# Kernel optimization log

Hardware: AMD Instinct MI355X
Metric: run time of the kernel (lower is better)

## Reference

```python
import jax, jax.numpy as jnp
import numpy as np

EPS = 1e-5  # matches `self.dist(f, pt) + 1e-05` in the torch module

N, D, P = 262144, 64, 256


def setup_inputs() -> dict:
    key = jax.random.key(0)
    k1, k2, k3 = jax.random.split(key, 3)
    features = jax.random.normal(k1, (N, D), dtype=jnp.float32)      # flattened boxes' feature vectors
    prototypes = jax.random.normal(k2, (P, D), dtype=jnp.float32)    # stacked self.prototypes.values()
    proto_labels = jax.random.randint(k3, (P,), 0, 1000)             # list(self.prototypes) keys
    return {"features": features, "prototypes": prototypes, "proto_labels": proto_labels}


def reference(features, prototypes, proto_labels):
    # F.mse_loss(f, pt) = mean((f - pt)**2) over the D feature dim.
    # Expand ||f - p||^2 = ||f||^2 - 2 f.p + ||p||^2 so we never materialize [N, P, D].
    d = features.shape[-1]
    f2 = jnp.sum(features * features, axis=-1, keepdims=True)          # [N, 1]
    p2 = jnp.sum(prototypes * prototypes, axis=-1)                     # [P]
    cross = features @ prototypes.T                                    # [N, P]
    mse = (f2 - 2.0 * cross + p2[None, :]) / d                         # [N, P] per-pair MSE
    inv_d = 1.0 / (mse + EPS)                                          # ds in the torch code
    labels = proto_labels[jnp.argmax(inv_d, axis=-1)]                  # box[-1] = fls[ds.argmax()]
    return inv_d, labels
```

## Files before the change

kernel.cpp:

```cpp
#include <hip/hip_runtime.h>


#define PROTOS 256
#define DIM 64
#define MARGIN 0.125f

__global__ __launch_bounds__(256, 4)
void protonet_kernel(const float* __restrict__ feats,
                     const float* __restrict__ protos,
                     const int* __restrict__ plabels,
                     float* __restrict__ out_inv,
                     float* __restrict__ out_lab,
                     int rows_total)
{
    const int p    = threadIdx.x;
    const int lane = threadIdx.x & 63;
    const int wid  = threadIdx.x >> 6;

    float pr[DIM];
    {
        const float4* prv = (const float4*)(protos + p * DIM);
        #pragma unroll
        for (int i = 0; i < DIM / 4; ++i) {
            float4 v = prv[i];
            pr[4 * i + 0] = v.x; pr[4 * i + 1] = v.y;
            pr[4 * i + 2] = v.z; pr[4 * i + 3] = v.w;
        }
    }
    double p2d = 0.0;
    #pragma unroll
    for (int k = 0; k < DIM; ++k) p2d = fma((double)pr[k], (double)pr[k], p2d);
    float p2f = (float)p2d;

    __shared__ unsigned int s_m1[4], s_m2[4];
    __shared__ double s_dval[4];
    __shared__ int    s_didx[4];
    __shared__ int    s_flag;

    for (int row = blockIdx.x; row < rows_total; row += gridDim.x) {
        const float* frow = feats + (size_t)row * DIM;
        const float4* f4  = (const float4*)frow;

        float fv  = frow[lane];
        float fsf = fv * fv;
        #pragma unroll
        for (int s = 32; s > 0; s >>= 1) fsf += __shfl_xor(fsf, s, 64);

        float a0 = 0.f, a1 = 0.f, a2 = 0.f, a3 = 0.f;
        #pragma unroll
        for (int i = 0; i < DIM / 4; ++i) {
            float4 x = f4[i];
            a0 = fmaf(x.x, pr[4 * i + 0], a0);
            a1 = fmaf(x.y, pr[4 * i + 1], a1);
            a2 = fmaf(x.z, pr[4 * i + 2], a2);
            a3 = fmaf(x.w, pr[4 * i + 3], a3);
        }
        float cross = (a0 + a1) + (a2 + a3);
        float msed  = fsf - 2.0f * cross + p2f;

        out_inv[(size_t)row * PROTOS + p] = 1.0f / (msed * (1.0f / 64.0f) + 1e-5f);

        unsigned int comb = (__float_as_uint(msed) & 0xFFFFFF00u) | (unsigned int)p;
        unsigned int m1 = comb;
        #pragma unroll
        for (int s = 32; s > 0; s >>= 1) {
            unsigned int o = __shfl_xor(m1, s, 64);
            m1 = (o < m1) ? o : m1;
        }
        unsigned int masked = (comb == m1) ? 0xFFFFFFFFu : comb;
        unsigned int m2 = masked;
        #pragma unroll
        for (int s = 32; s > 0; s >>= 1) {
            unsigned int o = __shfl_xor(m2, s, 64);
            m2 = (o < m2) ? o : m2;
        }
        if (lane == 0) { s_m1[wid] = m1; s_m2[wid] = m2; }
        __syncthreads();

        if (threadIdx.x == 0) {
            unsigned int b1 = 0xFFFFFFFFu, b2 = 0xFFFFFFFFu;
            #pragma unroll
            for (int w = 0; w < 4; ++w) {
                unsigned int u1 = s_m1[w], u2 = s_m2[w];
                unsigned int hi = (b1 > u1) ? b1 : u1;
                unsigned int lo2 = (b2 < u2) ? b2 : u2;
                b1 = (b1 < u1) ? b1 : u1;
                b2 = (hi < lo2) ? hi : lo2;
            }
            float v1 = __uint_as_float(b1 & 0xFFFFFF00u);
            float v2 = __uint_as_float(b2 & 0xFFFFFF00u);
            int resc = (v2 - v1) < MARGIN;
            s_flag = resc;
            if (!resc) out_lab[row] = (float)plabels[b1 & 0xFFu];
        }
        __syncthreads();

        if (s_flag) {
            float fl   = frow[lane];
            double fsd = (double)fl * (double)fl;
            #pragma unroll
            for (int s = 32; s > 0; s >>= 1) fsd += __shfl_xor(fsd, s, 64);

            double d0 = 0.0, d1 = 0.0, d2 = 0.0, d3 = 0.0;
            #pragma unroll
            for (int k = 0; k < DIM; k += 4) {
                d0 = fma((double)frow[k + 0], (double)pr[k + 0], d0);
                d1 = fma((double)frow[k + 1], (double)pr[k + 1], d1);
                d2 = fma((double)frow[k + 2], (double)pr[k + 2], d2);
                d3 = fma((double)frow[k + 3], (double)pr[k + 3], d3);
            }
            double crossd = (d0 + d1) + (d2 + d3);
            double msedd  = fsd - 2.0 * crossd + p2d;

            double bv = msedd;
            int    bi = p;
            #pragma unroll
            for (int s = 32; s > 0; s >>= 1) {
                double ov = __shfl_xor(bv, s, 64);
                int    oi = __shfl_xor(bi, s, 64);
                if (ov < bv || (ov == bv && oi < bi)) { bv = ov; bi = oi; }
            }
            if (lane == 0) { s_dval[wid] = bv; s_didx[wid] = bi; }
            __syncthreads();
            if (threadIdx.x == 0) {
                double v = s_dval[0];
                int    i = s_didx[0];
                #pragma unroll
                for (int w = 1; w < 4; ++w) {
                    if (s_dval[w] < v || (s_dval[w] == v && s_didx[w] < i)) {
                        v = s_dval[w]; i = s_didx[w];
                    }
                }
                out_lab[row] = (float)plabels[i];
            }
            __syncthreads();
        }
    }
}

extern "C" void kernel_launch(void* const* d_in, const int* in_sizes, int n_in,
                              void* d_out, int out_size, void* d_ws, size_t ws_size,
                              hipStream_t stream) {
    const float* feats  = (const float*)d_in[0];
    const float* protos = (const float*)d_in[1];
    const int*   plab   = (const int*)d_in[2];
    const int rows = in_sizes[0] / DIM;

    float* out_inv = (float*)d_out;
    float* out_lab = out_inv + (size_t)rows * PROTOS;

    dim3 grid(2048), block(256);
    hipLaunchKernelGGL(protonet_kernel, grid, block, 0, stream,
                       feats, protos, plab, out_inv, out_lab, rows);
}
```

Measured before the change: 737.4 us.

## Process four rows per block iteration with fused top-2 reduction

Each block now handles groups of four feature rows per loop iteration. Each prototype register is reused across four rows, the shuffle reductions of the four rows are interleaved, and the two barriers are shared by the whole group instead of paid per row. The two-pass min/second-min reduction is merged into one combined top-2 butterfly, and an asm barrier pins the prototype values in VGPRs. Launch bounds drop to 3 blocks per SM to make room for the extra registers, which lowers occupancy; a tail loop in block 0 handles leftover rows.

```diff
diff --git a/kernel.cpp b/kernel.cpp
--- a/kernel.cpp
+++ b/kernel.cpp
@@ -4,8 +4,146 @@
 #define PROTOS 256
 #define DIM 64
 #define MARGIN 0.125f
-
-__global__ __launch_bounds__(256, 4)
+#define RB 4
+
+template <int R>
+__device__ __forceinline__ void do_group(
+    int row0,
+    const float* __restrict__ feats,
+    const int* __restrict__ plabels,
+    float* __restrict__ out_inv,
+    float* __restrict__ out_lab,
+    const float (&pr)[DIM], double p2d, float p2f,
+    unsigned int (*s_m1)[4], unsigned int (*s_m2)[4],
+    int* s_resc, double* s_dval, int* s_didx)
+{
+    const int p    = threadIdx.x;
+    const int lane = threadIdx.x & 63;
+    const int wid  = threadIdx.x >> 6;
+
+    float fs[R];
+    #pragma unroll
+    for (int r = 0; r < R; ++r) {
+        float fv = feats[(size_t)(row0 + r) * DIM + lane];
+        fs[r] = fv * fv;
+    }
+    #pragma unroll
+    for (int s = 32; s > 0; s >>= 1) {
+        #pragma unroll
+        for (int r = 0; r < R; ++r) fs[r] += __shfl_xor(fs[r], s, 64);
+    }
+
+    float a[R][4];
+    #pragma unroll
+    for (int r = 0; r < R; ++r) { a[r][0] = a[r][1] = a[r][2] = a[r][3] = 0.f; }
+    #pragma unroll
+    for (int i = 0; i < DIM / 4; ++i) {
+        #pragma unroll
+        for (int r = 0; r < R; ++r) {
+            float4 x = ((const float4*)(feats + (size_t)(row0 + r) * DIM))[i];
+            a[r][0] = fmaf(x.x, pr[4 * i + 0], a[r][0]);
+            a[r][1] = fmaf(x.y, pr[4 * i + 1], a[r][1]);
+            a[r][2] = fmaf(x.z, pr[4 * i + 2], a[r][2]);
+            a[r][3] = fmaf(x.w, pr[4 * i + 3], a[r][3]);
+        }
+    }
+
+    unsigned int m1[R], m2[R];
+    #pragma unroll
+    for (int r = 0; r < R; ++r) {
+        float cross = (a[r][0] + a[r][1]) + (a[r][2] + a[r][3]);
+        float msed  = fs[r] - 2.0f * cross + p2f;
+        out_inv[(size_t)(row0 + r) * PROTOS + p] =
+            1.0f / (msed * (1.0f / 64.0f) + 1e-5f);
+        m1[r] = (__float_as_uint(msed) & 0xFFFFFF00u) | (unsigned int)p;
+        m2[r] = 0xFFFFFFFFu;
+    }
+
+    #pragma unroll
+    for (int s = 32; s > 0; s >>= 1) {
+        #pragma unroll
+        for (int r = 0; r < R; ++r) {
+            unsigned int o1 = __shfl_xor(m1[r], s, 64);
+            unsigned int o2 = __shfl_xor(m2[r], s, 64);
+            unsigned int hi  = (m1[r] > o1) ? m1[r] : o1;
+            unsigned int lo  = (m1[r] < o1) ? m1[r] : o1;
+            unsigned int mn2 = (m2[r] < o2) ? m2[r] : o2;
+            m1[r] = lo;
+            m2[r] = (hi < mn2) ? hi : mn2;
+        }
+    }
+    if (lane == 0) {
+        #pragma unroll
+        for (int r = 0; r < R; ++r) { s_m1[r][wid] = m1[r]; s_m2[r][wid] = m2[r]; }
+    }
+    __syncthreads();
+
+    if (threadIdx.x < R) {
+        const int r = threadIdx.x;
+        unsigned int b1 = 0xFFFFFFFFu, b2 = 0xFFFFFFFFu;
+        #pragma unroll
+        for (int w = 0; w < 4; ++w) {
+            unsigned int u1 = s_m1[r][w], u2 = s_m2[r][w];
+            unsigned int hi  = (b1 > u1) ? b1 : u1;
+            unsigned int lo2 = (b2 < u2) ? b2 : u2;
+            b1 = (b1 < u1) ? b1 : u1;
+            b2 = (hi < lo2) ? hi : lo2;
+        }
+        float v1 = __uint_as_float(b1 & 0xFFFFFF00u);
+        float v2 = __uint_as_float(b2 & 0xFFFFFF00u);
+        int resc = (v2 - v1) < MARGIN;
+        s_resc[r] = resc;
+        if (!resc) out_lab[row0 + r] = (float)plabels[b1 & 0xFFu];
+    }
+    __syncthreads();
+
+    for (int r = 0; r < R; ++r) {
+        if (!s_resc[r]) continue;
+        const int row = row0 + r;
+        const float* frow = feats + (size_t)row * DIM;
+
+        float fl   = frow[lane];
+        double fsd = (double)fl * (double)fl;
+        #pragma unroll
+        for (int s = 32; s > 0; s >>= 1) fsd += __shfl_xor(fsd, s, 64);
+
+        double d0 = 0.0, d1 = 0.0, d2 = 0.0, d3 = 0.0;
+        #pragma unroll
+        for (int k = 0; k < DIM; k += 4) {
+            d0 = fma((double)frow[k + 0], (double)pr[k + 0], d0);
+            d1 = fma((double)frow[k + 1], (double)pr[k + 1], d1);
+            d2 = fma((double)frow[k + 2], (double)pr[k + 2], d2);
+            d3 = fma((double)frow[k + 3], (double)pr[k + 3], d3);
+        }
+        double crossd = (d0 + d1) + (d2 + d3);
+        double msedd  = fsd - 2.0 * crossd + p2d;
+
+        double bv = msedd;
+        int    bi = p;
+        #pragma unroll
+        for (int s = 32; s > 0; s >>= 1) {
+            double ov = __shfl_xor(bv, s, 64);
+            int    oi = __shfl_xor(bi, s, 64);
+            if (ov < bv || (ov == bv && oi < bi)) { bv = ov; bi = oi; }
+        }
+        if (lane == 0) { s_dval[wid] = bv; s_didx[wid] = bi; }
+        __syncthreads();
+        if (threadIdx.x == 0) {
+            double v = s_dval[0];
+            int    i = s_didx[0];
+            #pragma unroll
+            for (int w = 1; w < 4; ++w) {
+                if (s_dval[w] < v || (s_dval[w] == v && s_didx[w] < i)) {
+                    v = s_dval[w]; i = s_didx[w];
+                }
+            }
+            out_lab[row] = (float)plabels[i];
+        }
+        __syncthreads();
+    }
+}
+
+__global__ __launch_bounds__(256, 3)
 void protonet_kernel(const float* __restrict__ feats,
                      const float* __restrict__ protos,
                      const int* __restrict__ plabels,
@@ -13,9 +151,7 @@
                      float* __restrict__ out_lab,
                      int rows_total)
 {
-    const int p    = threadIdx.x;
-    const int lane = threadIdx.x & 63;
-    const int wid  = threadIdx.x >> 6;
+    const int p = threadIdx.x;
 
     float pr[DIM];
     {
@@ -27,113 +163,29 @@
             pr[4 * i + 2] = v.z; pr[4 * i + 3] = v.w;
         }
     }
+    #pragma unroll
+    for (int k = 0; k < DIM; ++k) asm volatile("" : "+v"(pr[k]));
+
     double p2d = 0.0;
     #pragma unroll
     for (int k = 0; k < DIM; ++k) p2d = fma((double)pr[k], (double)pr[k], p2d);
     float p2f = (float)p2d;
 
-    __shared__ unsigned int s_m1[4], s_m2[4];
+    __shared__ unsigned int s_m1[RB][4], s_m2[RB][4];
+    __shared__ int    s_resc[RB];
     __shared__ double s_dval[4];
     __shared__ int    s_didx[4];
-    __shared__ int    s_flag;
-
-    for (int row = blockIdx.x; row < rows_total; row += gridDim.x) {
-        const float* frow = feats + (size_t)row * DIM;
-        const float4* f4  = (const float4*)frow;
-
-        float fv  = frow[lane];
-        float fsf = fv * fv;
-        #pragma unroll
-        for (int s = 32; s > 0; s >>= 1) fsf += __shfl_xor(fsf, s, 64);
-
-        float a0 = 0.f, a1 = 0.f, a2 = 0.f, a3 = 0.f;
-        #pragma unroll
-        for (int i = 0; i < DIM / 4; ++i) {
-            float4 x = f4[i];
-            a0 = fmaf(x.x, pr[4 * i + 0], a0);
-            a1 = fmaf(x.y, pr[4 * i + 1], a1);
-            a2 = fmaf(x.z, pr[4 * i + 2], a2);
-            a3 = fmaf(x.w, pr[4 * i + 3], a3);
-        }
-        float cross = (a0 + a1) + (a2 + a3);
-        float msed  = fsf - 2.0f * cross + p2f;
-
-        out_inv[(size_t)row * PROTOS + p] = 1.0f / (msed * (1.0f / 64.0f) + 1e-5f);
-
-        unsigned int comb = (__float_as_uint(msed) & 0xFFFFFF00u) | (unsigned int)p;
-        unsigned int m1 = comb;
-        #pragma unroll
-        for (int s = 32; s > 0; s >>= 1) {
-            unsigned int o = __shfl_xor(m1, s, 64);
-            m1 = (o < m1) ? o : m1;
-        }
-        unsigned int masked = (comb == m1) ? 0xFFFFFFFFu : comb;
-        unsigned int m2 = masked;
-        #pragma unroll
-        for (int s = 32; s > 0; s >>= 1) {
-            unsigned int o = __shfl_xor(m2, s, 64);
-            m2 = (o < m2) ? o : m2;
-        }
-        if (lane == 0) { s_m1[wid] = m1; s_m2[wid] = m2; }
-        __syncthreads();
-
-        if (threadIdx.x == 0) {
-            unsigned int b1 = 0xFFFFFFFFu, b2 = 0xFFFFFFFFu;
-            #pragma unroll
-            for (int w = 0; w < 4; ++w) {
-                unsigned int u1 = s_m1[w], u2 = s_m2[w];
-                unsigned int hi = (b1 > u1) ? b1 : u1;
-                unsigned int lo2 = (b2 < u2) ? b2 : u2;
-                b1 = (b1 < u1) ? b1 : u1;
-                b2 = (hi < lo2) ? hi : lo2;
-            }
-            float v1 = __uint_as_float(b1 & 0xFFFFFF00u);
-            float v2 = __uint_as_float(b2 & 0xFFFFFF00u);
-            int resc = (v2 - v1) < MARGIN;
-            s_flag = resc;
-            if (!resc) out_lab[row] = (float)plabels[b1 & 0xFFu];
-        }
-        __syncthreads();
-
-        if (s_flag) {
-            float fl   = frow[lane];
-            double fsd = (double)fl * (double)fl;
-            #pragma unroll
-            for (int s = 32; s > 0; s >>= 1) fsd += __shfl_xor(fsd, s, 64);
-
-            double d0 = 0.0, d1 = 0.0, d2 = 0.0, d3 = 0.0;
-            #pragma unroll
-            for (int k = 0; k < DIM; k += 4) {
-                d0 = fma((double)frow[k + 0], (double)pr[k + 0], d0);
-                d1 = fma((double)frow[k + 1], (double)pr[k + 1], d1);
-                d2 = fma((double)frow[k + 2], (double)pr[k + 2], d2);
-                d3 = fma((double)frow[k + 3], (double)pr[k + 3], d3);
-            }
-            double crossd = (d0 + d1) + (d2 + d3);
-            double msedd  = fsd - 2.0 * crossd + p2d;
-
-            double bv = msedd;
-            int    bi = p;
-            #pragma unroll
-            for (int s = 32; s > 0; s >>= 1) {
-                double ov = __shfl_xor(bv, s, 64);
-                int    oi = __shfl_xor(bi, s, 64);
-                if (ov < bv || (ov == bv && oi < bi)) { bv = ov; bi = oi; }
-            }
-            if (lane == 0) { s_dval[wid] = bv; s_didx[wid] = bi; }
-            __syncthreads();
-            if (threadIdx.x == 0) {
-                double v = s_dval[0];
-                int    i = s_didx[0];
-                #pragma unroll
-                for (int w = 1; w < 4; ++w) {
-                    if (s_dval[w] < v || (s_dval[w] == v && s_didx[w] < i)) {
-                        v = s_dval[w]; i = s_didx[w];
-                    }
-                }
-                out_lab[row] = (float)plabels[i];
-            }
-            __syncthreads();
+
+    const int ngroups = rows_total / RB;
+    for (int g = blockIdx.x; g < ngroups; g += gridDim.x) {
+        do_group<RB>(g * RB, feats, plabels, out_inv, out_lab,
+                     pr, p2d, p2f, s_m1, s_m2, s_resc, s_dval, s_didx);
+    }
+
+    if (blockIdx.x == 0) {
+        for (int row = ngroups * RB; row < rows_total; ++row) {
+            do_group<1>(row, feats, plabels, out_inv, out_lab,
+                        pr, p2d, p2f, s_m1, s_m2, s_resc, s_dval, s_didx);
         }
     }
 }
```

Result: faster. 709.3 us (-3.8%).

## Map one thread per row with prototypes in shared memory and per-warp rescoring

Applied to the files above, without the earlier changes.

Switches from one block per row (a thread per prototype) to a thread per feature row. Each thread loops over all 256 prototypes read from LDS with broadcast loads and tracks its own best and second-best distances, which removes the per-row block-wide shuffle reductions and __syncthreads. Near-tie rows are rescored in double precision cooperatively by the whole wavefront using a ballot loop. The reciprocal now uses a hardware rcp plus one Newton step. The trade-off is strided, uncoalesced float4 output stores across rows and heavy register pressure from the 64 feature values held per thread.

```diff
diff --git a/kernel.cpp b/kernel.cpp
--- a/kernel.cpp
+++ b/kernel.cpp
@@ -4,8 +4,9 @@
 #define PROTOS 256
 #define DIM 64
 #define MARGIN 0.125f
+#define BLOCK 512
 
-__global__ __launch_bounds__(256, 4)
+__global__ __launch_bounds__(BLOCK, 4)
 void protonet_kernel(const float* __restrict__ feats,
                      const float* __restrict__ protos,
                      const int* __restrict__ plabels,
@@ -13,127 +14,160 @@
                      float* __restrict__ out_lab,
                      int rows_total)
 {
-    const int p    = threadIdx.x;
-    const int lane = threadIdx.x & 63;
-    const int wid  = threadIdx.x >> 6;
+    __shared__ float  s_pr[PROTOS][DIM];
+    __shared__ float  s_p2f[PROTOS];
+    __shared__ double s_p2d[PROTOS];
 
-    float pr[DIM];
     {
-        const float4* prv = (const float4*)(protos + p * DIM);
+        const float4* src = (const float4*)protos;
+        float4* dst = (float4*)&s_pr[0][0];
+        #pragma unroll
+        for (int t = 0; t < (PROTOS * DIM / 4) / BLOCK; ++t)
+            dst[t * BLOCK + threadIdx.x] = src[t * BLOCK + threadIdx.x];
+    }
+    __syncthreads();
+
+    if (threadIdx.x < PROTOS) {
+        const int p = threadIdx.x;
+        const float4* q4 = (const float4*)&s_pr[p][0];
+        double acc = 0.0;
         #pragma unroll
         for (int i = 0; i < DIM / 4; ++i) {
-            float4 v = prv[i];
-            pr[4 * i + 0] = v.x; pr[4 * i + 1] = v.y;
-            pr[4 * i + 2] = v.z; pr[4 * i + 3] = v.w;
+            float4 q = q4[i];
+            acc = fma((double)q.x, (double)q.x, acc);
+            acc = fma((double)q.y, (double)q.y, acc);
+            acc = fma((double)q.z, (double)q.z, acc);
+            acc = fma((double)q.w, (double)q.w, acc);
         }
+        s_p2d[p] = acc;
+        s_p2f[p] = (float)acc;
     }
-    double p2d = 0.0;
-    #pragma unroll
-    for (int k = 0; k < DIM; ++k) p2d = fma((double)pr[k], (double)pr[k], p2d);
-    float p2f = (float)p2d;
+    __syncthreads();
 
-    __shared__ unsigned int s_m1[4], s_m2[4];
-    __shared__ double s_dval[4];
-    __shared__ int    s_didx[4];
-    __shared__ int    s_flag;
+    const int lane = threadIdx.x & 63;
+    const long long stride = (long long)gridDim.x * BLOCK;
 
-    for (int row = blockIdx.x; row < rows_total; row += gridDim.x) {
-        const float* frow = feats + (size_t)row * DIM;
-        const float4* f4  = (const float4*)frow;
+    for (long long row = (long long)blockIdx.x * BLOCK + threadIdx.x;
+         row - lane < (long long)rows_total;
+         row += stride)
+    {
+        const int valid = row < (long long)rows_total;
+        const long long rrow = valid ? row : (long long)(rows_total - 1);
+        const float* frow = feats + rrow * DIM;
 
-        float fv  = frow[lane];
-        float fsf = fv * fv;
+        float f[DIM];
+        {
+            const float4* f4 = (const float4*)frow;
+            #pragma unroll
+            for (int i = 0; i < DIM / 4; ++i) {
+                float4 v = f4[i];
+                f[4 * i + 0] = v.x; f[4 * i + 1] = v.y;
+                f[4 * i + 2] = v.z; f[4 * i + 3] = v.w;
+            }
+        }
         #pragma unroll
-        for (int s = 32; s > 0; s >>= 1) fsf += __shfl_xor(fsf, s, 64);
+        for (int k = 0; k < DIM; ++k) asm volatile("" : "+v"(f[k]));
 
-        float a0 = 0.f, a1 = 0.f, a2 = 0.f, a3 = 0.f;
+        float s0 = 0.f, s1 = 0.f, s2 = 0.f, s3 = 0.f;
         #pragma unroll
-        for (int i = 0; i < DIM / 4; ++i) {
-            float4 x = f4[i];
-            a0 = fmaf(x.x, pr[4 * i + 0], a0);
-            a1 = fmaf(x.y, pr[4 * i + 1], a1);
-            a2 = fmaf(x.z, pr[4 * i + 2], a2);
-            a3 = fmaf(x.w, pr[4 * i + 3], a3);
+        for (int k = 0; k < DIM; k += 4) {
+            s0 = fmaf(f[k + 0], f[k + 0], s0);
+            s1 = fmaf(f[k + 1], f[k + 1], s1);
+            s2 = fmaf(f[k + 2], f[k + 2], s2);
+            s3 = fmaf(f[k + 3], f[k + 3], s3);
         }
-        float cross = (a0 + a1) + (a2 + a3);
-        float msed  = fsf - 2.0f * cross + p2f;
+        const float fsf = (s0 + s1) + (s2 + s3);
 
-        out_inv[(size_t)row * PROTOS + p] = 1.0f / (msed * (1.0f / 64.0f) + 1e-5f);
+        float b1 = 3.4e38f, b2 = 3.4e38f;
+        int   bi = 0;
+        float iv0 = 0.f, iv1 = 0.f;
+        float* orow = out_inv + rrow * PROTOS;
 
-        unsigned int comb = (__float_as_uint(msed) & 0xFFFFFF00u) | (unsigned int)p;
-        unsigned int m1 = comb;
-        #pragma unroll
-        for (int s = 32; s > 0; s >>= 1) {
-            unsigned int o = __shfl_xor(m1, s, 64);
-            m1 = (o < m1) ? o : m1;
+        #pragma unroll 1
+        for (int p = 0; p < PROTOS; p += 2) {
+            const float4* q4 = (const float4*)&s_pr[p][0];
+            const float4* r4 = (const float4*)&s_pr[p + 1][0];
+            float a0 = 0.f, a1 = 0.f, a2 = 0.f, a3 = 0.f;
+            float c0 = 0.f, c1 = 0.f, c2 = 0.f, c3 = 0.f;
+            #pragma unroll
+            for (int i = 0; i < DIM / 4; ++i) {
+                float4 q = q4[i];
+                float4 r = r4[i];
+                a0 = fmaf(f[4 * i + 0], q.x, a0);
+                a1 = fmaf(f[4 * i + 1], q.y, a1);
+                a2 = fmaf(f[4 * i + 2], q.z, a2);
+                a3 = fmaf(f[4 * i + 3], q.w, a3);
+                c0 = fmaf(f[4 * i + 0], r.x, c0);
+                c1 = fmaf(f[4 * i + 1], r.y, c1);
+                c2 = fmaf(f[4 * i + 2], r.z, c2);
+                c3 = fmaf(f[4 * i + 3], r.w, c3);
+            }
+            float2 pp = *(const float2*)&s_p2f[p];
+            float cra = (a0 + a1) + (a2 + a3);
+            float crb = (c0 + c1) + (c2 + c3);
+            float m0 = fsf - 2.0f * cra + pp.x;
+            float m1 = fsf - 2.0f * crb + pp.y;
+
+            bi = (m0 < b1) ? p : bi;
+            float hi0 = fmaxf(b1, m0);
+            b1 = fminf(b1, m0);
+            b2 = fminf(b2, hi0);
+            bi = (m1 < b1) ? (p + 1) : bi;
+            float hi1 = fmaxf(b1, m1);
+            b1 = fminf(b1, m1);
+            b2 = fminf(b2, hi1);
+
+            float d0 = fmaf(m0, 0.015625f, 1e-5f);
+            float d1 = fmaf(m1, 0.015625f, 1e-5f);
+            float r0 = __builtin_amdgcn_rcpf(d0);
+            float r1 = __builtin_amdgcn_rcpf(d1);
+            r0 = r0 * (2.0f - d0 * r0);
+            r1 = r1 * (2.0f - d1 * r1);
+
+            if ((p & 2) == 0) { iv0 = r0; iv1 = r1; }
+            else if (valid) {
+                *(float4*)&orow[p - 2] = make_float4(iv0, iv1, r0, r1);
+            }
         }
-        unsigned int masked = (comb == m1) ? 0xFFFFFFFFu : comb;
-        unsigned int m2 = masked;
-        #pragma unroll
-        for (int s = 32; s > 0; s >>= 1) {
-            unsigned int o = __shfl_xor(m2, s, 64);
-            m2 = (o < m2) ? o : m2;
-        }
-        if (lane == 0) { s_m1[wid] = m1; s_m2[wid] = m2; }
-        __syncthreads();
 
-        if (threadIdx.x == 0) {
-            unsigned int b1 = 0xFFFFFFFFu, b2 = 0xFFFFFFFFu;
-            #pragma unroll
-            for (int w = 0; w < 4; ++w) {
-                unsigned int u1 = s_m1[w], u2 = s_m2[w];
-                unsigned int hi = (b1 > u1) ? b1 : u1;
-                unsigned int lo2 = (b2 < u2) ? b2 : u2;
-                b1 = (b1 < u1) ? b1 : u1;
-                b2 = (hi < lo2) ? hi : lo2;
-            }
-            float v1 = __uint_as_float(b1 & 0xFFFFFF00u);
-            float v2 = __uint_as_float(b2 & 0xFFFFFF00u);
-            int resc = (v2 - v1) < MARGIN;
-            s_flag = resc;
-            if (!resc) out_lab[row] = (float)plabels[b1 & 0xFFu];
-        }
-        __syncthreads();
+        const int resc = valid && ((b2 - b1) < MARGIN);
+        if (valid && !resc) out_lab[row] = (float)plabels[bi];
 
-        if (s_flag) {
-            float fl   = frow[lane];
+        unsigned long long bal = __ballot(resc);
+        while (bal) {
+            const int l = __builtin_ctzll(bal);
+            bal &= bal - 1;
+            const long long rw = (row - lane) + l;
+            const float* fr = feats + rw * DIM;
+
+            float fl = fr[lane];
             double fsd = (double)fl * (double)fl;
             #pragma unroll
             for (int s = 32; s > 0; s >>= 1) fsd += __shfl_xor(fsd, s, 64);
 
-            double d0 = 0.0, d1 = 0.0, d2 = 0.0, d3 = 0.0;
-            #pragma unroll
-            for (int k = 0; k < DIM; k += 4) {
-                d0 = fma((double)frow[k + 0], (double)pr[k + 0], d0);
-                d1 = fma((double)frow[k + 1], (double)pr[k + 1], d1);
-                d2 = fma((double)frow[k + 2], (double)pr[k + 2], d2);
-                d3 = fma((double)frow[k + 3], (double)pr[k + 3], d3);
+            double bv = 1e300; int bidx = 0;
+            #pragma unroll 1
+            for (int j = 0; j < 4; ++j) {
+                const int p = lane + 64 * j;
+                double d0 = 0.0, d1 = 0.0, d2 = 0.0, d3 = 0.0;
+                #pragma unroll
+                for (int k = 0; k < DIM; k += 4) {
+                    d0 = fma((double)fr[k + 0], (double)s_pr[p][k + 0], d0);
+                    d1 = fma((double)fr[k + 1], (double)s_pr[p][k + 1], d1);
+                    d2 = fma((double)fr[k + 2], (double)s_pr[p][k + 2], d2);
+                    d3 = fma((double)fr[k + 3], (double)s_pr[p][k + 3], d3);
+                }
+                double crossd = (d0 + d1) + (d2 + d3);
+                double msedd  = fsd - 2.0 * crossd + s_p2d[p];
+                if (msedd < bv) { bv = msedd; bidx = p; }
             }
-            double crossd = (d0 + d1) + (d2 + d3);
-            double msedd  = fsd - 2.0 * crossd + p2d;
-
-            double bv = msedd;
-            int    bi = p;
             #pragma unroll
             for (int s = 32; s > 0; s >>= 1) {
                 double ov = __shfl_xor(bv, s, 64);
-                int    oi = __shfl_xor(bi, s, 64);
-                if (ov < bv || (ov == bv && oi < bi)) { bv = ov; bi = oi; }
+                int    oi = __shfl_xor(bidx, s, 64);
+                if (ov < bv || (ov == bv && oi < bidx)) { bv = ov; bidx = oi; }
             }
-            if (lane == 0) { s_dval[wid] = bv; s_didx[wid] = bi; }
-            __syncthreads();
-            if (threadIdx.x == 0) {
-                double v = s_dval[0];
-                int    i = s_didx[0];
-                #pragma unroll
-                for (int w = 1; w < 4; ++w) {
-                    if (s_dval[w] < v || (s_dval[w] == v && s_didx[w] < i)) {
-                        v = s_dval[w]; i = s_didx[w];
-                    }
-                }
-                out_lab[row] = (float)plabels[i];
-            }
-            __syncthreads();
+            if (lane == 0) out_lab[rw] = (float)plabels[bidx];
         }
     }
 }
@@ -149,7 +183,7 @@
     float* out_inv = (float*)d_out;
     float* out_lab = out_inv + (size_t)rows * PROTOS;
 
-    dim3 grid(2048), block(256);
+    dim3 grid(512), block(BLOCK);
     hipLaunchKernelGGL(protonet_kernel, grid, block, 0, stream,
                        feats, protos, plab, out_inv, out_lab, rows);
 }
```

New measurement: 2.291 ms. +210.8%, slower.

## Batch eight rows per block iteration with single barrier and ballot-based ambiguity detection

Applied to the files above, without the earlier changes.

Each block now handles RB=8 rows per loop iteration. Feature norms are computed cooperatively and the per-row argmin reductions are batched, so two or three block barriers cover eight rows instead of several per row. The near-tie test uses a per-wave ballot on an offset key that leaves out the row norm, and the reciprocal uses rcp plus one Newton step. The launch-bounds occupancy hint drops to 2 to fit the extra registers, which risks lower occupancy, and the rescue path still runs serially per row.

```diff
diff --git a/kernel.cpp b/kernel.cpp
--- a/kernel.cpp
+++ b/kernel.cpp
@@ -4,8 +4,11 @@
 #define PROTOS 256
 #define DIM 64
 #define MARGIN 0.125f
+#define BLOCK 256
+#define RB 8
+#define TOFF 1024.0f
 
-__global__ __launch_bounds__(256, 4)
+__global__ __launch_bounds__(BLOCK, 2)
 void protonet_kernel(const float* __restrict__ feats,
                      const float* __restrict__ protos,
                      const int* __restrict__ plabels,
@@ -27,76 +30,116 @@
             pr[4 * i + 2] = v.z; pr[4 * i + 3] = v.w;
         }
     }
+    #pragma unroll
+    for (int k = 0; k < DIM; ++k) asm volatile("" : "+v"(pr[k]));
+
     double p2d = 0.0;
     #pragma unroll
     for (int k = 0; k < DIM; ++k) p2d = fma((double)pr[k], (double)pr[k], p2d);
-    float p2f = (float)p2d;
+    const float p2f   = (float)p2d;
+    const float p2pad = p2f + TOFF;
 
-    __shared__ unsigned int s_m1[4], s_m2[4];
-    __shared__ double s_dval[4];
-    __shared__ int    s_didx[4];
-    __shared__ int    s_flag;
+    __shared__ unsigned int s_m1[RB][4];
+    __shared__ unsigned int s_wfl[RB][4];
+    __shared__ float        s_fs[RB];
+    __shared__ int          s_resc[RB];
+    __shared__ double       s_dval[4];
+    __shared__ int          s_didx[4];
 
-    for (int row = blockIdx.x; row < rows_total; row += gridDim.x) {
-        const float* frow = feats + (size_t)row * DIM;
-        const float4* f4  = (const float4*)frow;
+    const long long nbatch = ((long long)rows_total + RB - 1) / RB;
+    for (long long b = blockIdx.x; b < nbatch; b += gridDim.x) {
+        const long long row0 = b * RB;
 
-        float fv  = frow[lane];
-        float fsf = fv * fv;
-        #pragma unroll
-        for (int s = 32; s > 0; s >>= 1) fsf += __shfl_xor(fsf, s, 64);
+        {
+            const int r = p >> 5;
+            const int e = (p & 31) * 2;
+            long long rr = row0 + r;
+            if (rr >= rows_total) rr = rows_total - 1;
+            float2 fv = *(const float2*)(feats + rr * DIM + e);
+            float s = fmaf(fv.x, fv.x, fv.y * fv.y);
+            #pragma unroll
+            for (int sh = 16; sh > 0; sh >>= 1) s += __shfl_xor(s, sh, 64);
+            if ((p & 31) == 0) s_fs[r] = s;
+        }
 
-        float a0 = 0.f, a1 = 0.f, a2 = 0.f, a3 = 0.f;
-        #pragma unroll
-        for (int i = 0; i < DIM / 4; ++i) {
-            float4 x = f4[i];
-            a0 = fmaf(x.x, pr[4 * i + 0], a0);
-            a1 = fmaf(x.y, pr[4 * i + 1], a1);
-            a2 = fmaf(x.z, pr[4 * i + 2], a2);
-            a3 = fmaf(x.w, pr[4 * i + 3], a3);
-        }
-        float cross = (a0 + a1) + (a2 + a3);
-        float msed  = fsf - 2.0f * cross + p2f;
+        float cross[RB];
+        #pragma unroll 4
+        for (int r = 0; r < RB; ++r) {
+            long long rr = row0 + r;
+            if (rr >= rows_total) rr = rows_total - 1;
+            const float4* f4 = (const float4*)(feats + rr * DIM);
+            float a0 = 0.f, a1 = 0.f, a2 = 0.f, a3 = 0.f;
+            #pragma unroll
+            for (int i = 0; i < DIM / 4; ++i) {
+                float4 x = f4[i];
+                a0 = fmaf(x.x, pr[4 * i + 0], a0);
+                a1 = fmaf(x.y, pr[4 * i + 1], a1);
+                a2 = fmaf(x.z, pr[4 * i + 2], a2);
+                a3 = fmaf(x.w, pr[4 * i + 3], a3);
+            }
+            float c = (a0 + a1) + (a2 + a3);
+            cross[r] = c;
 
-        out_inv[(size_t)row * PROTOS + p] = 1.0f / (msed * (1.0f / 64.0f) + 1e-5f);
-
-        unsigned int comb = (__float_as_uint(msed) & 0xFFFFFF00u) | (unsigned int)p;
-        unsigned int m1 = comb;
-        #pragma unroll
-        for (int s = 32; s > 0; s >>= 1) {
-            unsigned int o = __shfl_xor(m1, s, 64);
-            m1 = (o < m1) ? o : m1;
-        }
-        unsigned int masked = (comb == m1) ? 0xFFFFFFFFu : comb;
-        unsigned int m2 = masked;
-        #pragma unroll
-        for (int s = 32; s > 0; s >>= 1) {
-            unsigned int o = __shfl_xor(m2, s, 64);
-            m2 = (o < m2) ? o : m2;
-        }
-        if (lane == 0) { s_m1[wid] = m1; s_m2[wid] = m2; }
-        __syncthreads();
-
-        if (threadIdx.x == 0) {
-            unsigned int b1 = 0xFFFFFFFFu, b2 = 0xFFFFFFFFu;
+            float t = fmaxf(fmaf(c, -2.0f, p2pad), 0.0f);
+            unsigned int key = (__float_as_uint(t) & 0xFFFFFF00u) | (unsigned int)p;
+            unsigned int m1 = key;
             #pragma unroll
-            for (int w = 0; w < 4; ++w) {
-                unsigned int u1 = s_m1[w], u2 = s_m2[w];
-                unsigned int hi = (b1 > u1) ? b1 : u1;
-                unsigned int lo2 = (b2 < u2) ? b2 : u2;
-                b1 = (b1 < u1) ? b1 : u1;
-                b2 = (hi < lo2) ? hi : lo2;
+            for (int sh = 32; sh > 0; sh >>= 1) {
+                unsigned int o = __shfl_xor(m1, sh, 64);
+                m1 = (o < m1) ? o : m1;
             }
-            float v1 = __uint_as_float(b1 & 0xFFFFFF00u);
-            float v2 = __uint_as_float(b2 & 0xFFFFFF00u);
-            int resc = (v2 - v1) < MARGIN;
-            s_flag = resc;
-            if (!resc) out_lab[row] = (float)plabels[b1 & 0xFFu];
+            float tb = __uint_as_float(m1 & 0xFFFFFF00u);
+            unsigned long long bal = __ballot((t - tb) < MARGIN);
+            if (lane == 0) {
+                s_m1[r][wid]  = m1;
+                s_wfl[r][wid] = (__popcll(bal) >= 2) ? 1u : 0u;
+            }
         }
         __syncthreads();
 
-        if (s_flag) {
-            float fl   = frow[lane];
+        if (p < RB) {
+            const int r = p;
+            const long long rowg = row0 + r;
+            if (rowg < rows_total) {
+                unsigned int b1 = 0xFFFFFFFFu;
+                #pragma unroll
+                for (int w = 0; w < 4; ++w) {
+                    unsigned int u = s_m1[r][w];
+                    b1 = (u < b1) ? u : b1;
+                }
+                unsigned int m2 = 0xFFFFFFFFu, fl = 0;
+                #pragma unroll
+                for (int w = 0; w < 4; ++w) {
+                    unsigned int u = s_m1[r][w];
+                    if (u == b1) fl = s_wfl[r][w];
+                    else         m2 = (u < m2) ? u : m2;
+                }
+                float v1 = __uint_as_float(b1 & 0xFFFFFF00u);
+                float v2 = __uint_as_float(m2 & 0xFFFFFF00u);
+                int resc = fl || ((v2 - v1) < MARGIN);
+                s_resc[r] = resc;
+                if (!resc) out_lab[rowg] = (float)plabels[b1 & 0xFFu];
+            } else s_resc[r] = 0;
+        }
+
+        #pragma unroll
+        for (int r = 0; r < RB; ++r) {
+            const long long rowg = row0 + r;
+            float m = (s_fs[r] - 2.0f * cross[r]) + p2f;
+            float d = fmaf(m, 0.015625f, 1e-5f);
+            float rc = __builtin_amdgcn_rcpf(d);
+            rc = rc * (2.0f - d * rc);
+            if (rowg < rows_total) out_inv[rowg * PROTOS + p] = rc;
+        }
+        __syncthreads();
+
+        #pragma unroll 1
+        for (int r = 0; r < RB; ++r) {
+            if (!s_resc[r]) continue;
+            const long long rw = row0 + r;
+            const float* fr = feats + rw * DIM;
+
+            float fl = fr[lane];
             double fsd = (double)fl * (double)fl;
             #pragma unroll
             for (int s = 32; s > 0; s >>= 1) fsd += __shfl_xor(fsd, s, 64);
@@ -104,10 +147,10 @@
             double d0 = 0.0, d1 = 0.0, d2 = 0.0, d3 = 0.0;
             #pragma unroll
             for (int k = 0; k < DIM; k += 4) {
-                d0 = fma((double)frow[k + 0], (double)pr[k + 0], d0);
-                d1 = fma((double)frow[k + 1], (double)pr[k + 1], d1);
-                d2 = fma((double)frow[k + 2], (double)pr[k + 2], d2);
-                d3 = fma((double)frow[k + 3], (double)pr[k + 3], d3);
+                d0 = fma((double)fr[k + 0], (double)pr[k + 0], d0);
+                d1 = fma((double)fr[k + 1], (double)pr[k + 1], d1);
+                d2 = fma((double)fr[k + 2], (double)pr[k + 2], d2);
+                d3 = fma((double)fr[k + 3], (double)pr[k + 3], d3);
             }
             double crossd = (d0 + d1) + (d2 + d3);
             double msedd  = fsd - 2.0 * crossd + p2d;
@@ -131,7 +174,7 @@
                         v = s_dval[w]; i = s_didx[w];
                     }
                 }
-                out_lab[row] = (float)plabels[i];
+                out_lab[rw] = (float)plabels[i];
             }
             __syncthreads();
         }
@@ -149,7 +192,7 @@
     float* out_inv = (float*)d_out;
     float* out_lab = out_inv + (size_t)rows * PROTOS;
 
-    dim3 grid(2048), block(256);
+    dim3 grid(2048), block(BLOCK);
     hipLaunchKernelGGL(protonet_kernel, grid, block, 0, stream,
                        feats, protos, plab, out_inv, out_lab, rows);
 }
```

After: 784.5 us. 1.06x slower.
